# Kernel optimization log

Hardware: AMD Instinct MI355X
Metric: run time of the kernel (lower is better)

Reference implementation:

```python
import jax, jax.numpy as jnp
import numpy as np

N_EMBED = 1024
NUM_EXPERTS = 8
TOP_K = 2
D_FF = 4 * N_EMBED
B, S = 4, 2048


def setup_inputs() -> dict:
    key = jax.random.key(0)
    ks = jax.random.split(key, 8)
    s = 0.02
    return {
        "x": jax.random.normal(ks[0], (B, S, N_EMBED), jnp.float32),
        "noise": jax.random.normal(ks[1], (B, S, NUM_EXPERTS), jnp.float32),
        "w_route": jax.random.normal(ks[2], (N_EMBED, NUM_EXPERTS), jnp.float32) * s,
        "b_route": jnp.zeros((NUM_EXPERTS,), jnp.float32),
        "w_noise": jax.random.normal(ks[3], (N_EMBED, NUM_EXPERTS), jnp.float32) * s,
        "b_noise": jnp.zeros((NUM_EXPERTS,), jnp.float32),
        "w1": jax.random.normal(ks[4], (NUM_EXPERTS, N_EMBED, D_FF), jnp.float32) * s,
        "b1": jnp.zeros((NUM_EXPERTS, D_FF), jnp.float32),
        "w2": jax.random.normal(ks[5], (NUM_EXPERTS, D_FF, N_EMBED), jnp.float32) * s,
        "b2": jnp.zeros((NUM_EXPERTS, N_EMBED), jnp.float32),
    }


def reference(x, noise, w_route, b_route, w_noise, b_noise, w1, b1, w2, b2):
    # NoisyTopkRouter: logits + N(0,1)*softplus(noise_logits), top-k, softmax
    # over a sparse (-inf filled) logit matrix -> gates are exactly 0 for
    # non-selected experts.
    logits = x @ w_route + b_route                                   # [B,S,E]
    noise_logits = x @ w_noise + b_noise                             # [B,S,E]
    noisy = logits + noise * jax.nn.softplus(noise_logits)           # [B,S,E]
    _, topi = jax.lax.top_k(noisy, TOP_K)                            # [B,S,k]
    sel = jax.nn.one_hot(topi, NUM_EXPERTS, dtype=bool).any(-2)      # [B,S,E]
    sparse_logits = jnp.where(sel, noisy, -jnp.inf)
    gates = jax.nn.softmax(sparse_logits, axis=-1)                   # [B,S,E]

    T = x.shape[0] * x.shape[1]
    xf = x.reshape(T, N_EMBED)                                       # [T,d]
    gf = gates.reshape(T, NUM_EXPERTS)                               # [T,E]

    # Dense per-expert MLP weighted by gates; gate==0 for unselected tokens,
    # so this matches the masked gather/scatter of the original exactly.
    out = jnp.zeros_like(xf)
    for e in range(NUM_EXPERTS):
        h = jax.nn.relu(xf @ w1[e] + b1[e])                          # [T,4d]
        y = h @ w2[e] + b2[e]                                        # [T,d]
        out = out + y * gf[:, e:e + 1]
    return out.reshape(x.shape)
```

## Files before the change

### kernel.cpp

```cpp
#include <hip/hip_runtime.h>

typedef __bf16 bf16_t;
typedef __bf16 bf16x8 __attribute__((ext_vector_type(8)));
typedef __bf16 bf16x4 __attribute__((ext_vector_type(4)));
typedef float  f32x4  __attribute__((ext_vector_type(4)));

#define T_TOK 8192
#define DIM   1024
#define DFF   4096
#define NEXP  8

__device__ __forceinline__ void gll16(const void* g, void* l) {
    __builtin_amdgcn_global_load_lds(
        (const __attribute__((address_space(1))) char*)g,
        (__attribute__((address_space(3))) char*)l, 16, 0, 0);
}

__device__ __forceinline__ void transpose_tile(
    const float* __restrict__ src, bf16_t* __restrict__ dst,
    int R, int C, int r0, int c0, int tid, float (*t)[65])
{
    {
        int cg = tid & 15, r = tid >> 4;
#pragma unroll
        for (int i = 0; i < 4; ++i) {
            int rr = r + i * 16;
            float4 v = *(const float4*)&src[(size_t)(r0 + rr) * C + c0 + cg * 4];
            t[rr][cg * 4 + 0] = v.x; t[rr][cg * 4 + 1] = v.y;
            t[rr][cg * 4 + 2] = v.z; t[rr][cg * 4 + 3] = v.w;
        }
    }
    __syncthreads();
    {
        int rr = tid & 7, c = tid >> 3;
#pragma unroll
        for (int i = 0; i < 2; ++i) {
            int cc = c + i * 32;
            bf16x8 o;
#pragma unroll
            for (int j = 0; j < 8; ++j) o[j] = (bf16_t)t[rr * 8 + j][cc];
            *(bf16x8*)&dst[(size_t)(c0 + cc) * R + r0 + rr * 8] = o;
        }
    }
}

__global__ __launch_bounds__(256) void fused_pre_kernel(
    const float* __restrict__ x, const float* __restrict__ noise,
    const float* __restrict__ w_route, const float* __restrict__ b_route,
    const float* __restrict__ w_noise, const float* __restrict__ b_noise,
    const float* __restrict__ w1, const float* __restrict__ w2,
    bf16_t* __restrict__ w1t, bf16_t* __restrict__ w2t,
    int* __restrict__ counts, int* __restrict__ lists, float* __restrict__ gate_tok)
{
    __shared__ float t[64][65];
    int id = blockIdx.x;
    int tid = threadIdx.x;

    if (id >= 2048) {
        if (id < 10240) {
            int t1 = id - 2048;
            int e = t1 >> 10, rem = t1 & 1023;
            int bx = rem & 63, by = rem >> 6;
            transpose_tile(w1 + (size_t)e * DIM * DFF, w1t + (size_t)e * DIM * DFF,
                           DIM, DFF, by * 64, bx * 64, tid, t);
        } else {
            int t2 = id - 10240;
            int e = t2 >> 10, rem = t2 & 1023;
            int bx = rem & 15, by = rem >> 4;
            transpose_tile(w2 + (size_t)e * DFF * DIM, w2t + (size_t)e * DFF * DIM,
                           DFF, DIM, by * 64, bx * 64, tid, t);
        }
        return;
    }

    int wave = tid >> 6;
    int lane = tid & 63;
    int tok = id * 4 + wave;
    if (tok >= T_TOK) return;

    const float* xr = x + (size_t)tok * DIM;
    double aR[NEXP], aN[NEXP];
#pragma unroll
    for (int e = 0; e < NEXP; ++e) { aR[e] = 0.0; aN[e] = 0.0; }

#pragma unroll 4
    for (int i = 0; i < 16; ++i) {
        int k = lane + i * 64;
        double xv = (double)xr[k];
        const float4* wr4 = (const float4*)(w_route + (size_t)k * 8);
        const float4* wn4 = (const float4*)(w_noise + (size_t)k * 8);
        float4 r0 = wr4[0], r1 = wr4[1];
        float4 n0 = wn4[0], n1 = wn4[1];
        aR[0] += xv * (double)r0.x; aR[1] += xv * (double)r0.y;
        aR[2] += xv * (double)r0.z; aR[3] += xv * (double)r0.w;
        aR[4] += xv * (double)r1.x; aR[5] += xv * (double)r1.y;
        aR[6] += xv * (double)r1.z; aR[7] += xv * (double)r1.w;
        aN[0] += xv * (double)n0.x; aN[1] += xv * (double)n0.y;
        aN[2] += xv * (double)n0.z; aN[3] += xv * (double)n0.w;
        aN[4] += xv * (double)n1.x; aN[5] += xv * (double)n1.y;
        aN[6] += xv * (double)n1.z; aN[7] += xv * (double)n1.w;
    }
#pragma unroll
    for (int e = 0; e < NEXP; ++e) {
        for (int s = 1; s < 64; s <<= 1) {
            aR[e] += __shfl_xor(aR[e], s);
            aN[e] += __shfl_xor(aN[e], s);
        }
    }
    if (lane == 0) {
        double nv[NEXP];
#pragma unroll
        for (int e = 0; e < NEXP; ++e) {
            double lg = aR[e] + (double)b_route[e];
            double nl = aN[e] + (double)b_noise[e];
            double sp = (nl > 30.0) ? nl : log1p(exp(nl));
            nv[e] = lg + (double)noise[(size_t)tok * 8 + e] * sp;
        }
        int i1 = 0;
#pragma unroll
        for (int e = 1; e < NEXP; ++e) if (nv[e] > nv[i1]) i1 = e;
        int i2 = (i1 == 0) ? 1 : 0;
#pragma unroll
        for (int e = 0; e < NEXP; ++e) if (e != i1 && nv[e] > nv[i2]) i2 = e;
        double m = nv[i1];
        double e2 = exp(nv[i2] - m);
        double s = 1.0 + e2;
        gate_tok[2 * tok + 0] = (float)(1.0 / s);
        gate_tok[2 * tok + 1] = (float)(e2 / s);
        int p1 = atomicAdd(&counts[i1], 1);
        lists[i1 * T_TOK + p1] = 2 * tok + 0;
        int p2 = atomicAdd(&counts[i2], 1);
        lists[i2 * T_TOK + p2] = 2 * tok + 1;
    }
}

__global__ void prefix_kernel(const int* __restrict__ counts, int* __restrict__ bases) {
    if (threadIdx.x == 0 && blockIdx.x == 0) {
        int s = 0;
#pragma unroll
        for (int e = 0; e < NEXP; ++e) { bases[e] = s; s += counts[e]; }
    }
}

__global__ __launch_bounds__(256) void pack_a_kernel(
    const float* __restrict__ x, const int* __restrict__ bases,
    const int* __restrict__ lists, bf16_t* __restrict__ Ap, int* __restrict__ inv)
{
    int wave = threadIdx.x >> 6, lane = threadIdx.x & 63;
    int p = blockIdx.x * 4 + wave;
    int e = 0;
#pragma unroll
    for (int i = 1; i < NEXP; ++i) e += (p >= bases[i]);
    int pos = p - bases[e];
    int entry = lists[e * T_TOK + pos];
    if (lane == 0) inv[entry] = p;
    const float4* src = (const float4*)(x + (size_t)(entry >> 1) * DIM);
    bf16x4* dst = (bf16x4*)(Ap + (size_t)p * DIM);
#pragma unroll
    for (int j = 0; j < 4; ++j) {
        float4 v = src[lane + j * 64];
        bf16x4 o;
        o[0] = (bf16_t)v.x; o[1] = (bf16_t)v.y; o[2] = (bf16_t)v.z; o[3] = (bf16_t)v.w;
        dst[lane + j * 64] = o;
    }
}

template<int K, int MODE>
__global__ __launch_bounds__(256) void moe_gemm_kernel(
    const bf16_t* __restrict__ Asrc, const bf16_t* __restrict__ Wt,
    const float* __restrict__ bias,
    const int* __restrict__ counts, const int* __restrict__ bases,
    const int* __restrict__ lists, const float* __restrict__ gate_tok,
    bf16_t* __restrict__ Hout, bf16_t* __restrict__ Yp)
{
    constexpr int N = (MODE == 0) ? DFF : DIM;
    constexpr int NT = K / 64;
    constexpr int NY = N / 128;

    int wg = blockIdx.x + 64 * (blockIdx.y + NY * blockIdx.z);
    int e = wg & 7;
    int inner = wg >> 3;
    int xi = inner & 63;
    int yi = inner >> 6;

    int cnt = counts[e];
    int m0 = xi * 128;
    if (m0 >= cnt) return;
    int base = bases[e];
    int n0 = yi * 128;
    const int* list = lists + e * T_TOK;
    const bf16_t* W = Wt + (size_t)e * N * K;

    __shared__ __attribute__((aligned(16))) bf16_t Ah0[128 * 64];
    __shared__ __attribute__((aligned(16))) bf16_t Bh0[128 * 64];
    __shared__ __attribute__((aligned(16))) bf16_t Ah1[128 * 64];
    __shared__ __attribute__((aligned(16))) bf16_t Bh1[128 * 64];

    int tid = threadIdx.x;
    int lane = tid & 63;
    int wave = tid >> 6;
    int wr = wave >> 1, wc = wave & 1;

    int kcs = (((lane & 7) ^ (lane >> 3)) << 3);
    const bf16_t* pA[4];
    const bf16_t* pB[4];
#pragma unroll
    for (int i = 0; i < 4; ++i) {
        int c = wave * 4 + i;
        int r = c * 8 + (lane >> 3);
        int ridx = m0 + r; if (ridx > cnt - 1) ridx = cnt - 1;
        pA[i] = Asrc + (size_t)(base + ridx) * K + kcs;
        pB[i] = W + (size_t)(n0 + r) * K + kcs;
    }

    f32x4 acc[4][4];
#pragma unroll
    for (int m = 0; m < 4; ++m)
#pragma unroll
        for (int n = 0; n < 4; ++n)
            acc[m][n] = (f32x4){0.f, 0.f, 0.f, 0.f};

    int g = lane >> 4, ln15 = lane & 15, ln7 = lane & 7;

#define STAGE(An, Bn, k0) do {                                               \
    _Pragma("unroll") for (int i = 0; i < 4; ++i) {                          \
        int c = wave * 4 + i;                                                \
        gll16(pA[i] + (k0), (An) + c * 512);                                 \
        gll16(pB[i] + (k0), (Bn) + c * 512);                                 \
    } } while (0)

#define COMPUTE(Ab, Bb) do {                                                 \
    _Pragma("unroll") for (int kk = 0; kk < 2; ++kk) {                       \
        bf16x8 a[4], b[4];                                                   \
        int sw = (((kk * 4 + g) ^ ln7) << 3);                                \
        _Pragma("unroll") for (int n = 0; n < 4; ++n)                        \
            b[n] = *(const bf16x8*)((Bb) + (wc * 64 + n * 16 + ln15) * 64 + sw); \
        _Pragma("unroll") for (int m = 0; m < 4; ++m)                        \
            a[m] = *(const bf16x8*)((Ab) + (wr * 64 + m * 16 + ln15) * 64 + sw); \
        __builtin_amdgcn_s_setprio(1);                                       \
        _Pragma("unroll") for (int m = 0; m < 4; ++m)                        \
            _Pragma("unroll") for (int n = 0; n < 4; ++n)                    \
                acc[m][n] = __builtin_amdgcn_mfma_f32_16x16x32_bf16(a[m], b[n], acc[m][n], 0, 0, 0); \
        __builtin_amdgcn_s_setprio(0);                                       \
    } } while (0)

#define FENCE() __builtin_amdgcn_sched_barrier(0)
#define WAITV(n) asm volatile("s_waitcnt vmcnt(" #n ")" ::: "memory")

    STAGE(Ah0, Bh0, 0);

    for (int kt = 0; kt < NT; kt += 2) {
        if (kt + 1 < NT) { STAGE(Ah1, Bh1, (kt + 1) * 64); WAITV(8); }
        else             { WAITV(0); }
        FENCE(); __builtin_amdgcn_s_barrier(); FENCE();
        COMPUTE(Ah0, Bh0);
        FENCE(); __builtin_amdgcn_s_barrier(); FENCE();
        if (kt + 2 < NT) { STAGE(Ah0, Bh0, (kt + 2) * 64); WAITV(8); }
        else             { WAITV(0); }
        FENCE(); __builtin_amdgcn_s_barrier(); FENCE();
        COMPUTE(Ah1, Bh1);
        FENCE(); __builtin_amdgcn_s_barrier(); FENCE();
    }
#undef STAGE
#undef COMPUTE
#undef FENCE
#undef WAITV

    int l4 = lane >> 4;
    float bs[4];
#pragma unroll
    for (int n = 0; n < 4; ++n)
        bs[n] = bias[e * N + n0 + wc * 64 + n * 16 + ln15];
#pragma unroll
    for (int m = 0; m < 4; ++m) {
#pragma unroll
        for (int j = 0; j < 4; ++j) {
            int grow = m0 + wr * 64 + m * 16 + l4 * 4 + j;
            if (grow >= cnt) continue;
            if constexpr (MODE == 0) {
#pragma unroll
                for (int n = 0; n < 4; ++n) {
                    int gcol = n0 + wc * 64 + n * 16 + ln15;
                    float v = acc[m][n][j] + bs[n];
                    Hout[(size_t)(base + grow) * DFF + gcol] = (bf16_t)fmaxf(v, 0.f);
                }
            } else {
                float gt = gate_tok[list[grow]];
#pragma unroll
                for (int n = 0; n < 4; ++n) {
                    int gcol = n0 + wc * 64 + n * 16 + ln15;
                    Yp[(size_t)(base + grow) * DIM + gcol] = (bf16_t)(gt * (acc[m][n][j] + bs[n]));
                }
            }
        }
    }
}

__global__ __launch_bounds__(256) void combine_kernel(
    const bf16_t* __restrict__ Yp, const int* __restrict__ inv,
    float* __restrict__ out)
{
#pragma unroll
    for (int q = 0; q < 2; ++q) {
        int t = blockIdx.x * 2 + q;
        int p0 = inv[2 * t], p1 = inv[2 * t + 1];
        const bf16x4* a = (const bf16x4*)(Yp + (size_t)p0 * DIM);
        const bf16x4* b = (const bf16x4*)(Yp + (size_t)p1 * DIM);
        float4* o = (float4*)(out + (size_t)t * DIM);
        int i = threadIdx.x;
        bf16x4 va = a[i], vb = b[i];
        o[i] = make_float4((float)va[0] + (float)vb[0], (float)va[1] + (float)vb[1],
                           (float)va[2] + (float)vb[2], (float)va[3] + (float)vb[3]);
    }
}

extern "C" void kernel_launch(void* const* d_in, const int* in_sizes, int n_in,
                              void* d_out, int out_size, void* d_ws, size_t ws_size,
                              hipStream_t stream) {
    const float* x       = (const float*)d_in[0];
    const float* noise   = (const float*)d_in[1];
    const float* w_route = (const float*)d_in[2];
    const float* b_route = (const float*)d_in[3];
    const float* w_noise = (const float*)d_in[4];
    const float* b_noise = (const float*)d_in[5];
    const float* w1      = (const float*)d_in[6];
    const float* b1      = (const float*)d_in[7];
    const float* w2      = (const float*)d_in[8];
    const float* b2      = (const float*)d_in[9];
    float* out = (float*)d_out;

    char* ws = (char*)d_ws;
    size_t off = 0;
    auto alloc = [&](size_t bytes) {
        off = (off + 255) & ~(size_t)255;
        size_t r = off; off += bytes; return r;
    };
    int*    counts   = (int*)   (ws + alloc(32));
    int*    bases    = (int*)   (ws + alloc(32));
    int*    lists    = (int*)   (ws + alloc((size_t)NEXP * T_TOK * 4));
    float*  gate_tok = (float*) (ws + alloc((size_t)T_TOK * 2 * 4));
    int*    inv      = (int*)   (ws + alloc((size_t)T_TOK * 2 * 4));
    bf16_t* w1t      = (bf16_t*)(ws + alloc((size_t)NEXP * DFF * DIM * 2));
    bf16_t* w2t      = (bf16_t*)(ws + alloc((size_t)NEXP * DIM * DFF * 2));
    bf16_t* Ap       = (bf16_t*)(ws + alloc((size_t)T_TOK * 2 * DIM * 2));
    bf16_t* H        = (bf16_t*)(ws + alloc((size_t)T_TOK * 2 * DFF * 2));
    bf16_t* Yp       = w1t;
    (void)ws_size; (void)in_sizes; (void)n_in; (void)out_size;

    hipMemsetAsync(counts, 0, 32, stream);

    fused_pre_kernel<<<18432, 256, 0, stream>>>(x, noise, w_route, b_route, w_noise, b_noise,
                                                w1, w2, w1t, w2t, counts, lists, gate_tok);

    prefix_kernel<<<1, 64, 0, stream>>>(counts, bases);
    pack_a_kernel<<<T_TOK * 2 / 4, 256, 0, stream>>>(x, bases, lists, Ap, inv);

    moe_gemm_kernel<DIM, 0><<<dim3(64, DFF / 128, NEXP), 256, 0, stream>>>(
        Ap, w1t, b1, counts, bases, lists, gate_tok, H, nullptr);
    moe_gemm_kernel<DFF, 1><<<dim3(64, DIM / 128, NEXP), 256, 0, stream>>>(
        H, w2t, b2, counts, bases, lists, gate_tok, nullptr, Yp);

    combine_kernel<<<T_TOK / 2, 256, 0, stream>>>(Yp, inv, out);
}
```

Before: 742.1 us.

## Pre-tile transposed expert weights into contiguous 128x64 blocks for GEMM loads

The weight transpose now writes w1/w2 directly into a tiled layout where each 128-row by 64-k block is contiguous (8192 bf16), and the GEMM B-pointer indexing follows that layout so each k-step reads one contiguous 16 KB chunk. The transpose also switches from many 64x64 tile blocks to fewer blocks that each process a 64-row band in 128-column strips, cutting the pre-kernel grid from 18432 to 3072 blocks. The aim is more contiguous, DRAM-page-friendly weight streaming in the GEMMs and less block-launch overhead in the transpose. The risks are reduced parallelism in the transpose and a GEMM that now depends on the yi tile index being consistent with the new layout.

```diff
diff --git a/kernel.cpp b/kernel.cpp
--- a/kernel.cpp
+++ b/kernel.cpp
@@ -3,7 +3,10 @@
 typedef __bf16 bf16_t;
 typedef __bf16 bf16x8 __attribute__((ext_vector_type(8)));
 typedef __bf16 bf16x4 __attribute__((ext_vector_type(4)));
+typedef __bf16 bf16x2 __attribute__((ext_vector_type(2)));
 typedef float  f32x4  __attribute__((ext_vector_type(4)));
+typedef unsigned int u32;
+typedef u32 u32x4 __attribute__((ext_vector_type(4)));
 
 #define T_TOK 8192
 #define DIM   1024
@@ -16,31 +19,37 @@
         (__attribute__((address_space(3))) char*)l, 16, 0, 0);
 }
 
-__device__ __forceinline__ void transpose_tile(
+__device__ __forceinline__ void transpose_band(
     const float* __restrict__ src, bf16_t* __restrict__ dst,
-    int R, int C, int r0, int c0, int tid, float (*t)[65])
-{
-    {
-        int cg = tid & 15, r = tid >> 4;
-#pragma unroll
-        for (int i = 0; i < 4; ++i) {
-            int rr = r + i * 16;
-            float4 v = *(const float4*)&src[(size_t)(r0 + rr) * C + c0 + cg * 4];
-            t[rr][cg * 4 + 0] = v.x; t[rr][cg * 4 + 1] = v.y;
-            t[rr][cg * 4 + 2] = v.z; t[rr][cg * 4 + 3] = v.w;
-        }
-    }
-    __syncthreads();
-    {
-        int rr = tid & 7, c = tid >> 3;
-#pragma unroll
-        for (int i = 0; i < 2; ++i) {
-            int cc = c + i * 32;
-            bf16x8 o;
-#pragma unroll
-            for (int j = 0; j < 8; ++j) o[j] = (bf16_t)t[rr * 8 + j][cc];
-            *(bf16x8*)&dst[(size_t)(c0 + cc) * R + r0 + rr * 8] = o;
-        }
+    int Kw, int Nw, int k0, int nq, int tk, int tid, float* lds)
+{
+#pragma unroll 1
+    for (int s = 0; s < 8; ++s) {
+        int ns = nq + s * 128;
+#pragma unroll
+        for (int i = 0; i < 8; ++i) {
+            int r = i * 8 + (tid >> 5);
+            f32x4 v = *(const f32x4*)&src[(size_t)(k0 + r) * Nw + ns + (tid & 31) * 4];
+            *(f32x4*)&lds[r * 129 + (tid & 31) * 4] = v;
+        }
+        __syncthreads();
+        int tn = (nq >> 7) + s;
+        bf16_t* tile = dst + ((size_t)tn * (Kw >> 6) + tk) * 8192;
+#pragma unroll
+        for (int u = 0; u < 4; ++u) {
+            int id = u * 256 + tid;
+            int n = id >> 3, kc = id & 7;
+            u32 w[4];
+#pragma unroll
+            for (int j = 0; j < 4; ++j) {
+                union { bf16x2 h; u32 v; } cv;
+                cv.h[0] = (bf16_t)lds[(kc * 8 + j * 2 + 0) * 129 + n];
+                cv.h[1] = (bf16_t)lds[(kc * 8 + j * 2 + 1) * 129 + n];
+                w[j] = cv.v;
+            }
+            *(u32x4*)&tile[(size_t)n * 64 + kc * 8] = *(u32x4*)w;
+        }
+        __syncthreads();
     }
 }
 
@@ -52,23 +61,22 @@
     bf16_t* __restrict__ w1t, bf16_t* __restrict__ w2t,
     int* __restrict__ counts, int* __restrict__ lists, float* __restrict__ gate_tok)
 {
-    __shared__ float t[64][65];
+    __shared__ float lds[64 * 129];
     int id = blockIdx.x;
     int tid = threadIdx.x;
 
     if (id >= 2048) {
-        if (id < 10240) {
-            int t1 = id - 2048;
-            int e = t1 >> 10, rem = t1 & 1023;
-            int bx = rem & 63, by = rem >> 6;
-            transpose_tile(w1 + (size_t)e * DIM * DFF, w1t + (size_t)e * DIM * DFF,
-                           DIM, DFF, by * 64, bx * 64, tid, t);
+        int id2 = id - 2048;
+        if (id2 < 512) {
+            int e = id2 >> 6, rem = id2 & 63;
+            int b = rem >> 2, q = rem & 3;
+            transpose_band(w1 + (size_t)e * DIM * DFF, w1t + (size_t)e * DIM * DFF,
+                           DIM, DFF, b * 64, q * 1024, b, tid, lds);
         } else {
-            int t2 = id - 10240;
-            int e = t2 >> 10, rem = t2 & 1023;
-            int bx = rem & 15, by = rem >> 4;
-            transpose_tile(w2 + (size_t)e * DFF * DIM, w2t + (size_t)e * DFF * DIM,
-                           DFF, DIM, by * 64, bx * 64, tid, t);
+            int id3 = id2 - 512;
+            int e = id3 >> 6, b = id3 & 63;
+            transpose_band(w2 + (size_t)e * DFF * DIM, w2t + (size_t)e * DFF * DIM,
+                           DFF, DIM, b * 64, 0, b, tid, lds);
         }
         return;
     }
@@ -210,7 +218,7 @@
         int r = c * 8 + (lane >> 3);
         int ridx = m0 + r; if (ridx > cnt - 1) ridx = cnt - 1;
         pA[i] = Asrc + (size_t)(base + ridx) * K + kcs;
-        pB[i] = W + (size_t)(n0 + r) * K + kcs;
+        pB[i] = W + (size_t)yi * (K >> 6) * 8192 + (size_t)r * 64 + kcs;
     }
 
     f32x4 acc[4][4];
@@ -222,11 +230,11 @@
 
     int g = lane >> 4, ln15 = lane & 15, ln7 = lane & 7;
 
-#define STAGE(An, Bn, k0) do {                                               \
+#define STAGE(An, Bn, kA, kB) do {                                           \
     _Pragma("unroll") for (int i = 0; i < 4; ++i) {                          \
         int c = wave * 4 + i;                                                \
-        gll16(pA[i] + (k0), (An) + c * 512);                                 \
-        gll16(pB[i] + (k0), (Bn) + c * 512);                                 \
+        gll16(pA[i] + (kA), (An) + c * 512);                                 \
+        gll16(pB[i] + (kB), (Bn) + c * 512);                                 \
     } } while (0)
 
 #define COMPUTE(Ab, Bb) do {                                                 \
@@ -247,15 +255,15 @@
 #define FENCE() __builtin_amdgcn_sched_barrier(0)
 #define WAITV(n) asm volatile("s_waitcnt vmcnt(" #n ")" ::: "memory")
 
-    STAGE(Ah0, Bh0, 0);
+    STAGE(Ah0, Bh0, 0, 0);
 
     for (int kt = 0; kt < NT; kt += 2) {
-        if (kt + 1 < NT) { STAGE(Ah1, Bh1, (kt + 1) * 64); WAITV(8); }
+        if (kt + 1 < NT) { STAGE(Ah1, Bh1, (kt + 1) * 64, (size_t)(kt + 1) * 8192); WAITV(8); }
         else             { WAITV(0); }
         FENCE(); __builtin_amdgcn_s_barrier(); FENCE();
         COMPUTE(Ah0, Bh0);
         FENCE(); __builtin_amdgcn_s_barrier(); FENCE();
-        if (kt + 2 < NT) { STAGE(Ah0, Bh0, (kt + 2) * 64); WAITV(8); }
+        if (kt + 2 < NT) { STAGE(Ah0, Bh0, (kt + 2) * 64, (size_t)(kt + 2) * 8192); WAITV(8); }
         else             { WAITV(0); }
         FENCE(); __builtin_amdgcn_s_barrier(); FENCE();
         COMPUTE(Ah1, Bh1);
@@ -349,8 +357,8 @@
 
     hipMemsetAsync(counts, 0, 32, stream);
 
-    fused_pre_kernel<<<18432, 256, 0, stream>>>(x, noise, w_route, b_route, w_noise, b_noise,
-                                                w1, w2, w1t, w2t, counts, lists, gate_tok);
+    fused_pre_kernel<<<3072, 256, 0, stream>>>(x, noise, w_route, b_route, w_noise, b_noise,
+                                               w1, w2, w1t, w2t, counts, lists, gate_tok);
 
     prefix_kernel<<<1, 64, 0, stream>>>(counts, bases);
     pack_a_kernel<<<T_TOK * 2 / 4, 256, 0, stream>>>(x, bases, lists, Ap, inv);
```

After: 762.9 us. +2.8%, slower.
